# Kernel tuning notes

Hardware: AMD Instinct MI355X
Metric: run time of the kernel (lower is better)

Reference implementation:

```python
import jax, jax.numpy as jnp
import numpy as np

KS = 11                      # kernel_size from init_kwargs
HALF = (KS - 1) // 2         # half kernel for padding


def setup_inputs() -> dict:
    key = jax.random.key(0)
    k1, k2 = jax.random.split(key)
    x = jax.random.normal(k1, (1, 3, 720, 1280), dtype=jnp.float32)
    k = jax.random.normal(k2, (1, KS * KS, 720, 1280), dtype=jnp.float32)
    return {"x": x, "k": k, "padding": 1, "padding_value": 0}


def reference(x, k, padding, padding_value):
    # x: (b, c, hx, wx); k: (b, ks^2, h, w) pixel-wise kernels
    b, ks2, h, w = k.shape
    assert ks2 == KS * KS
    if padding:
        # padding=True branch: hx == h, wx == w; pad with padding_value
        xp = jnp.pad(x, ((0, 0), (0, 0), (HALF, HALF), (HALF, HALF)),
                     constant_values=float(padding_value))
    else:
        xp = x  # hx == h + KS - 1, wx == w + KS - 1
    # Accumulate shifted-view * per-pixel-weight products directly, never
    # materializing the (b, ks^2, c, h, w) stack the torch code builds.
    y = jnp.zeros((x.shape[0], x.shape[1], h, w), dtype=x.dtype)
    idx = 0
    for ii in range(KS):
        for jj in range(KS):
            # (b,c,h,w) shifted window * (b,1,h,w) kernel weight
            y = y + xp[:, :, ii:ii + h, jj:jj + w] * k[:, idx][:, None]
            idx += 1
    return y
```

## Files before the change

kernel.cpp:

```cpp
#include <hip/hip_runtime.h>


#define KS   11
#define HALF 5
#define H    720
#define W    1280
#define C    3
#define HW   (H * W)

__global__ __launch_bounds__(256) void apply_pixelwise_conv(
    const float* __restrict__ x,
    const float* __restrict__ k,
    float* __restrict__ out)
{
    const int quadsPerRow = W / 4;
    const int nQuads      = H * quadsPerRow;
    const int tid = blockIdx.x * blockDim.x + threadIdx.x;
    if (tid >= nQuads) return;

    const int h  = tid / quadsPerRow;
    const int w4 = (tid - h * quadsPerRow) * 4;
    const int kbase = h * W + w4;

    float acc[C][4];
    #pragma unroll
    for (int c = 0; c < C; ++c)
        #pragma unroll
        for (int p = 0; p < 4; ++p) acc[c][p] = 0.f;

    for (int ii = 0; ii < KS; ++ii) {
        const int  xr       = h + ii - HALF;
        const bool rowValid = (xr >= 0) & (xr < H);
        const int  rowOff   = xr * W;

        float xv[C][KS + 3];
        #pragma unroll
        for (int c = 0; c < C; ++c) {
            #pragma unroll
            for (int j = 0; j < KS + 3; ++j) {
                const int  xc = w4 - HALF + j;
                const bool ok = rowValid & (xc >= 0) & (xc < W);
                xv[c][j] = ok ? x[c * HW + rowOff + xc] : 0.f;
            }
        }

        #pragma unroll
        for (int jj = 0; jj < KS; ++jj) {
            const float4 kv = *reinterpret_cast<const float4*>(
                k + (size_t)(ii * KS + jj) * HW + kbase);
            #pragma unroll
            for (int c = 0; c < C; ++c) {
                acc[c][0] = fmaf(xv[c][jj + 0], kv.x, acc[c][0]);
                acc[c][1] = fmaf(xv[c][jj + 1], kv.y, acc[c][1]);
                acc[c][2] = fmaf(xv[c][jj + 2], kv.z, acc[c][2]);
                acc[c][3] = fmaf(xv[c][jj + 3], kv.w, acc[c][3]);
            }
        }
    }

    #pragma unroll
    for (int c = 0; c < C; ++c) {
        float4 o;
        o.x = acc[c][0]; o.y = acc[c][1]; o.z = acc[c][2]; o.w = acc[c][3];
        *reinterpret_cast<float4*>(out + c * HW + kbase) = o;
    }
}

extern "C" void kernel_launch(void* const* d_in, const int* in_sizes, int n_in,
                              void* d_out, int out_size, void* d_ws, size_t ws_size,
                              hipStream_t stream) {
    const float* x = (const float*)d_in[0];
    const float* k = (const float*)d_in[1];
    float* out = (float*)d_out;

    const int nQuads = H * (W / 4);
    const int block  = 256;
    const int grid   = (nQuads + block - 1) / block;
    apply_pixelwise_conv<<<grid, block, 0, stream>>>(x, k, out);
}
```

Measured before the change: 623.1 us.

## Stage input halo tile in shared memory and read with vector LDS loads

```diff
diff --git a/kernel.cpp b/kernel.cpp
--- a/kernel.cpp
+++ b/kernel.cpp
@@ -8,19 +8,38 @@
 #define C    3
 #define HW   (H * W)
 
+#define TW   64
+#define TH   16
+#define XW   (TW + 2 * HALF + 2)
+#define XH   (TH + 2 * HALF)
+#define NSTAGE (C * XH * XW)
+
 __global__ __launch_bounds__(256) void apply_pixelwise_conv(
     const float* __restrict__ x,
     const float* __restrict__ k,
     float* __restrict__ out)
 {
-    const int quadsPerRow = W / 4;
-    const int nQuads      = H * quadsPerRow;
-    const int tid = blockIdx.x * blockDim.x + threadIdx.x;
-    if (tid >= nQuads) return;
+    __shared__ float xs[C][XH][XW];
 
-    const int h  = tid / quadsPerRow;
-    const int w4 = (tid - h * quadsPerRow) * 4;
-    const int kbase = h * W + w4;
+    const int tx = threadIdx.x & 15;
+    const int ty = threadIdx.x >> 4;
+    const int w0 = (blockIdx.x % (W / TW)) * TW;
+    const int h0 = (blockIdx.x / (W / TW)) * TH;
+
+    #pragma unroll 1
+    for (int idx = threadIdx.x; idx < NSTAGE; idx += 256) {
+        const int c   = idx / (XH * XW);
+        const int rem = idx - c * (XH * XW);
+        const int r   = rem / XW;
+        const int col = rem - r * XW;
+        const int xr  = h0 - HALF + r;
+        const int xc  = w0 - HALF + col;
+        float v = 0.f;
+        if (col < TW + 2 * HALF && xr >= 0 && xr < H && xc >= 0 && xc < W)
+            v = x[c * HW + xr * W + xc];
+        xs[c][r][col] = v;
+    }
+    __syncthreads();
 
     float acc[C][4];
     #pragma unroll
@@ -28,20 +47,22 @@
         #pragma unroll
         for (int p = 0; p < 4; ++p) acc[c][p] = 0.f;
 
+    const int kbase = (h0 + ty) * W + w0 + tx * 4;
+
+    #pragma unroll 1
     for (int ii = 0; ii < KS; ++ii) {
-        const int  xr       = h + ii - HALF;
-        const bool rowValid = (xr >= 0) & (xr < H);
-        const int  rowOff   = xr * W;
-
         float xv[C][KS + 3];
         #pragma unroll
         for (int c = 0; c < C; ++c) {
-            #pragma unroll
-            for (int j = 0; j < KS + 3; ++j) {
-                const int  xc = w4 - HALF + j;
-                const bool ok = rowValid & (xc >= 0) & (xc < W);
-                xv[c][j] = ok ? x[c * HW + rowOff + xc] : 0.f;
-            }
+            const float* rowp = &xs[c][ty + ii][tx * 4];
+            const float4 a = *reinterpret_cast<const float4*>(rowp);
+            const float4 b = *reinterpret_cast<const float4*>(rowp + 4);
+            const float4 d = *reinterpret_cast<const float4*>(rowp + 8);
+            const float2 e = *reinterpret_cast<const float2*>(rowp + 12);
+            xv[c][0] = a.x;  xv[c][1] = a.y;  xv[c][2]  = a.z;  xv[c][3]  = a.w;
+            xv[c][4] = b.x;  xv[c][5] = b.y;  xv[c][6]  = b.z;  xv[c][7]  = b.w;
+            xv[c][8] = d.x;  xv[c][9] = d.y;  xv[c][10] = d.z;  xv[c][11] = d.w;
+            xv[c][12] = e.x; xv[c][13] = e.y;
         }
 
         #pragma unroll
@@ -73,8 +94,6 @@
     const float* k = (const float*)d_in[1];
     float* out = (float*)d_out;
 
-    const int nQuads = H * (W / 4);
-    const int block  = 256;
-    const int grid   = (nQuads + block - 1) / block;
-    apply_pixelwise_conv<<<grid, block, 0, stream>>>(x, k, out);
+    const int grid = (W / TW) * (H / TH);
+    apply_pixelwise_conv<<<grid, 256, 0, stream>>>(x, k, out);
 }
```

Result: faster. 596.9 us (-4.2%).
